# Kernel optimization log

Hardware: AMD Instinct MI355X
Metric: run time of the kernel (lower is better)

Reference implementation:

```python
import jax, jax.numpy as jnp
import numpy as np
import math

DIM = 2048
N_HEADS = 16
HEAD_DIM = DIM // N_HEADS  # 128
SEQ = 2048
EPS = 1e-5
NEG = -1e9


def get_slopes(n):
    # n is a power of 2 here (16)
    start = 2.0 ** (-2.0 ** (-(math.log2(n) - 3)))
    return [start * start ** i for i in range(n)]


def setup_inputs() -> dict:
    key = jax.random.key(0)
    ks = jax.random.split(key, 6)
    x = jax.random.normal(ks[0], (1, SEQ, DIM), dtype=jnp.float32)
    # causal additive mask (large negative above diagonal)
    causal = jnp.tril(jnp.ones((SEQ, SEQ), dtype=bool))
    mask = jnp.where(causal, 0.0, NEG).astype(jnp.float32)[None, None]
    scale_w = 0.02
    wq = jax.random.normal(ks[1], (DIM, DIM), dtype=jnp.float32) * scale_w  # [in, out]
    wk = jax.random.normal(ks[2], (DIM, DIM), dtype=jnp.float32) * scale_w
    wv = jax.random.normal(ks[3], (DIM, DIM), dtype=jnp.float32) * scale_w
    wo = jax.random.normal(ks[4], (DIM, DIM), dtype=jnp.float32) * scale_w
    # AttentionPrior params: shape_init=1, scale_init='slope' (stored as log), loc_init=0
    shape = jnp.ones((1, N_HEADS, 1, 1), dtype=jnp.float32)
    scale = jnp.log(jnp.asarray(get_slopes(N_HEADS), dtype=jnp.float32)).reshape(1, N_HEADS, 1, 1)
    loc = jnp.zeros((1, N_HEADS, 1, 1), dtype=jnp.float32)
    return {"x": x, "mask": mask, "wq": wq, "wk": wk, "wv": wv, "wo": wo,
            "shape": shape, "scale": scale, "loc": loc, "start_pos": 0}


def _prior_bias(shape, scale, loc, seqlen, start_pos):
    q_pos = jnp.arange(seqlen, dtype=jnp.float32) + start_pos
    k_pos = jnp.arange(seqlen + start_pos, dtype=jnp.float32)
    dist = (k_pos[None, :] - q_pos[:, None])[None, None]  # [1,1,S,K]
    loc_t = jnp.exp(loc) - jnp.exp(-loc)
    z = (dist - loc_t) * jnp.exp(scale)  # [1,H,S,K]
    return -(jnp.abs(z) + EPS) ** shape


def reference(x, mask, wq, wk, wv, wo, shape, scale, loc, start_pos):
    bsz, seqlen, _ = x.shape
    q = (x @ wq).reshape(bsz, seqlen, N_HEADS, HEAD_DIM)
    k = (x @ wk).reshape(bsz, seqlen, N_HEADS, HEAD_DIM)
    v = (x @ wv).reshape(bsz, seqlen, N_HEADS, HEAD_DIM)
    # start_pos=0 prefill: cache slice == current keys/values
    scores = jnp.einsum('bqhd,bkhd->bhqk', q, k) / math.sqrt(HEAD_DIM)
    scores = scores + _prior_bias(shape, scale, loc, seqlen, start_pos)
    scores = scores + mask
    probs = jax.nn.softmax(scores.astype(jnp.float32), axis=-1).astype(q.dtype)
    out = jnp.einsum('bhqk,bkhd->bqhd', probs, v).reshape(bsz, seqlen, DIM)
    return out @ wo
```

## Files before the change

kernel.cpp:

```cpp
#include <hip/hip_runtime.h>
#include <hip/hip_bf16.h>
#include <stdint.h>


typedef unsigned short u16;
typedef unsigned int u32;

using bf16x8 = __attribute__((ext_vector_type(8))) __bf16;
using f32x4  = __attribute__((ext_vector_type(4))) float;

__device__ __forceinline__ u16 f2bf(float f) {
  union { float f; u32 u; } v; v.f = f;
  u32 r = (v.u + 0x7FFFu + ((v.u >> 16) & 1u)) >> 16;
  return (u16)r;
}

__device__ __forceinline__ void gload16(const void* g, void* l) {
  __builtin_amdgcn_global_load_lds((const __attribute__((address_space(1))) void*)g,
                                   (__attribute__((address_space(3))) void*)l, 16, 0, 0);
}

__device__ __forceinline__ int cumchunks(int qt) {
  if (qt < 8)  return qt;
  if (qt < 16) return 8 + 2 * (qt - 8);
  if (qt < 24) return 24 + 3 * (qt - 16);
  return 48 + 4 * (qt - 24);
}

__global__ __launch_bounds__(256) void convx(const float* __restrict__ x, u16* __restrict__ xb) {
  int i = blockIdx.x * 256 + threadIdx.x;
  float4 v = ((const float4*)x)[i];
  ushort4 o;
  o.x = f2bf(v.x); o.y = f2bf(v.y); o.z = f2bf(v.z); o.w = f2bf(v.w);
  ((ushort4*)xb)[i] = o;
}

__global__ __launch_bounds__(256) void transw(const float* __restrict__ wq, const float* __restrict__ wk,
                                              const float* __restrict__ wv, const float* __restrict__ wo,
                                              u16* __restrict__ wqkt, u16* __restrict__ wvt,
                                              u16* __restrict__ wot) {
  __shared__ float tile[32][33];
  const int z = blockIdx.z;
  const float* src = (z == 0) ? wq : (z == 1) ? wk : (z == 2) ? wv : wo;
  u16* dst = (z == 0) ? wqkt : (z == 1) ? (wqkt + 2048 * 2048) : (z == 2) ? wvt : wot;
  const int c0 = blockIdx.x * 32, r0 = blockIdx.y * 32;
  const int t = threadIdx.x;
  const int ci = t & 31, rj = t >> 5;
#pragma unroll
  for (int j = 0; j < 4; ++j)
    tile[rj + j * 8][ci] = src[(size_t)(r0 + rj + j * 8) * 2048 + c0 + ci];
  __syncthreads();
#pragma unroll
  for (int j = 0; j < 4; ++j) {
    int rr = rj + j * 8;
    dst[(size_t)(c0 + rr) * 2048 + r0 + ci] = f2bf(tile[ci][rr]);
  }
}

template <int OUTF32>
__global__ __launch_bounds__(256) void gemm_bt(const u16* __restrict__ A, const u16* __restrict__ Bt,
                                               void* __restrict__ Cv, int M, int N, int K,
                                               float scl, int scl_cols) {
  __shared__ u16 lds[16384];
  const int t = threadIdx.x;
  const int w = t >> 6, l = t & 63;
  const int bn = blockIdx.x, bm = blockIdx.y;
  const int wm = w >> 1, wn = w & 1;
  const int lrow = l & 15, lgrp = l >> 4;

  f32x4 acc[4][4] = {};

  for (int k0 = 0; k0 < K; k0 += 64) {
    if (k0) __syncthreads();
#pragma unroll
    for (int p = 0; p < 4; ++p) {
      int i = (p * 4 + w) * 64 + l;
      int r = i >> 3, u = i & 7;
      const u16* src = A + (size_t)(bm * 128 + r) * K + k0 + ((u ^ (r & 7)) << 3);
      gload16(src, (char*)lds + (p * 4 + w) * 1024);
    }
#pragma unroll
    for (int p = 0; p < 4; ++p) {
      int i = (p * 4 + w) * 64 + l;
      int r = i >> 3, u = i & 7;
      const u16* src = Bt + (size_t)(bn * 128 + r) * K + k0 + ((u ^ (r & 7)) << 3);
      gload16(src, (char*)lds + 16384 + (p * 4 + w) * 1024);
    }
    __syncthreads();

#pragma unroll
    for (int kc = 0; kc < 2; ++kc) {
      bf16x8 af[4], bfr[4];
#pragma unroll
      for (int mt = 0; mt < 4; ++mt) {
        int rho = wm * 64 + mt * 16 + lrow;
        int un = (kc * 4 + lgrp) ^ (rho & 7);
        af[mt] = *(const bf16x8*)((const char*)lds + rho * 128 + un * 16);
      }
#pragma unroll
      for (int nt = 0; nt < 4; ++nt) {
        int rho = wn * 64 + nt * 16 + lrow;
        int un = (kc * 4 + lgrp) ^ (rho & 7);
        bfr[nt] = *(const bf16x8*)((const char*)lds + 16384 + rho * 128 + un * 16);
      }
#pragma unroll
      for (int mt = 0; mt < 4; ++mt)
#pragma unroll
        for (int nt = 0; nt < 4; ++nt)
          acc[mt][nt] = __builtin_amdgcn_mfma_f32_16x16x32_bf16(af[mt], bfr[nt], acc[mt][nt], 0, 0, 0);
    }
  }

  const int row0 = bm * 128 + wm * 64;
  const int col0 = bn * 128 + wn * 64;
#pragma unroll
  for (int mt = 0; mt < 4; ++mt)
#pragma unroll
    for (int nt = 0; nt < 4; ++nt) {
      int col = col0 + nt * 16 + lrow;
      float s = (col < scl_cols) ? scl : 1.0f;
#pragma unroll
      for (int r = 0; r < 4; ++r) {
        int row = row0 + mt * 16 + lgrp * 4 + r;
        float v = acc[mt][nt][r] * s;
        if (OUTF32) ((float*)Cv)[(size_t)row * N + col] = v;
        else        ((u16*)Cv)[(size_t)row * N + col] = f2bf(v);
      }
    }
}

__global__ __launch_bounds__(256) void attn_part(const u16* __restrict__ QK, const u16* __restrict__ Vt,
                                                 float* __restrict__ Opart, float* __restrict__ Lpart,
                                                 const float* __restrict__ g_shape,
                                                 const float* __restrict__ g_scale,
                                                 const float* __restrict__ g_loc,
                                                 const int* __restrict__ g_sp) {
  __shared__ u16 k_lds[2][8192];
  __shared__ u16 v_lds[2][8192];
  __shared__ u16 p_lds[4][1152];

  const int bid = blockIdx.x;
  const int h = bid / 80;
  const int rem = bid - h * 80;
  int qt, ch;
  if (rem < 8)       { qt = rem;                 ch = 0; }
  else if (rem < 24) { int r2 = rem - 8;  qt = 8  + (r2 >> 1); ch = r2 & 1; }
  else if (rem < 48) { int r3 = rem - 24; qt = 16 + r3 / 3;    ch = r3 - 3 * (r3 / 3); }
  else               { int r4 = rem - 48; qt = 24 + (r4 >> 2); ch = r4 & 3; }
  const int pid = bid;

  const int t = threadIdx.x, w = t >> 6, l = t & 63;
  const int lrow = l & 15, lgrp = l >> 4;

  const float sh = g_shape[h];
  const float es = __expf(g_scale[h]);
  const float lcv = g_loc[h];
  const float loc_t = __expf(lcv) - __expf(-lcv);
  const int sp = g_sp[0];
  const bool shape1 = (sh == 1.0f);

  const int qbase = qt * 64 + w * 16;

  bf16x8 qf[4];
  {
    const u16* qp = QK + (size_t)(qbase + lrow) * 4096 + h * 128 + lgrp * 8;
#pragma unroll
    for (int kc = 0; kc < 4; ++kc) qf[kc] = *(const bf16x8*)(qp + kc * 32);
  }

  f32x4 o[8] = {};
  float lr[4] = {0.0f, 0.0f, 0.0f, 0.0f};

  const int kstart = ch * 8;
  const int kend = min(kstart + 8, qt + 1);

#define STAGE_TILE(buf, kt_) do {                                                        \
    const int kv0s = (kt_) * 64;                                                         \
    _Pragma("unroll")                                                                    \
    for (int p = 0; p < 4; ++p) {                                                        \
      int i = (p * 4 + w) * 64 + l;                                                      \
      int r = i >> 4, u = i & 15;                                                        \
      const u16* src = QK + (size_t)(kv0s + r) * 4096 + 2048 + h * 128 + ((u ^ (r & 7)) << 3); \
      gload16(src, (char*)k_lds[buf] + (p * 4 + w) * 1024);                              \
    }                                                                                    \
    _Pragma("unroll")                                                                    \
    for (int p = 0; p < 4; ++p) {                                                        \
      int i = (p * 4 + w) * 64 + l;                                                      \
      int r = i >> 3, u = i & 7;                                                         \
      const u16* src = Vt + (size_t)(h * 128 + r) * 2048 + kv0s + ((u ^ (r & 7)) << 3);  \
      gload16(src, (char*)v_lds[buf] + (p * 4 + w) * 1024);                              \
    }                                                                                    \
  } while (0)

  STAGE_TILE(0, kstart);
  __syncthreads();

  for (int kt = kstart; kt < kend; ++kt) {
    const int cur = (kt - kstart) & 1;
    if (kt + 1 < kend) STAGE_TILE(cur ^ 1, kt + 1);
    const int kv0 = kt * 64;

    f32x4 s4[4];
#pragma unroll
    for (int nc = 0; nc < 4; ++nc) s4[nc] = f32x4{-11.0f, -11.0f, -11.0f, -11.0f};
#pragma unroll
    for (int kc = 0; kc < 4; ++kc) {
#pragma unroll
      for (int nc = 0; nc < 4; ++nc) {
        int rho = nc * 16 + lrow;
        int un = (kc * 4 + lgrp) ^ (rho & 7);
        bf16x8 bk = *(const bf16x8*)((const char*)k_lds[cur] + rho * 256 + un * 16);
        s4[nc] = __builtin_amdgcn_mfma_f32_16x16x32_bf16(qf[kc], bk, s4[nc], 0, 0, 0);
      }
    }

    f32x4 p4[4];
    const bool need_mask = (kv0 + 63 > qbase + sp);
    if (shape1 && !need_mask) {
#pragma unroll
      for (int r = 0; r < 4; ++r) {
        const float fb = (float)(kv0 + lrow - (qbase + lgrp * 4 + r) - sp) - loc_t;
#pragma unroll
        for (int nc = 0; nc < 4; ++nc) {
          float u = fb + (float)(nc * 16);
          float p = __expf(fmaf(-es, fabsf(u), s4[nc][r]));
          p4[nc][r] = p;
          lr[r] += p;
        }
      }
    } else if (shape1) {
#pragma unroll
      for (int r = 0; r < 4; ++r) {
        const float fb = (float)(kv0 + lrow - (qbase + lgrp * 4 + r) - sp) - loc_t;
#pragma unroll
        for (int nc = 0; nc < 4; ++nc) {
          float u = fb + (float)(nc * 16);
          float p = __expf(fmaf(-es, fabsf(u), s4[nc][r]));
          p = (u + loc_t > 0.0f) ? 0.0f : p;
          p4[nc][r] = p;
          lr[r] += p;
        }
      }
    } else {
#pragma unroll
      for (int r = 0; r < 4; ++r) {
        const float fb = (float)(kv0 + lrow - (qbase + lgrp * 4 + r) - sp) - loc_t;
#pragma unroll
        for (int nc = 0; nc < 4; ++nc) {
          float u = fb + (float)(nc * 16);
          float az = fmaf(es, fabsf(u), 1e-5f);
          float p = __expf(s4[nc][r] - __powf(az, sh));
          p = (u + loc_t > 0.0f) ? 0.0f : p;
          p4[nc][r] = p;
          lr[r] += p;
        }
      }
    }

#pragma unroll
    for (int r = 0; r < 4; ++r)
#pragma unroll
      for (int nc = 0; nc < 4; ++nc)
        p_lds[w][(lgrp * 4 + r) * 72 + nc * 16 + lrow] = f2bf(p4[nc][r]);

#pragma unroll
    for (int ks = 0; ks < 2; ++ks) {
      bf16x8 pa = *(const bf16x8*)((const char*)p_lds[w] + lrow * 144 + ks * 64 + lgrp * 16);
#pragma unroll
      for (int dc = 0; dc < 8; ++dc) {
        int rho = dc * 16 + lrow;
        int un = (ks * 4 + lgrp) ^ (rho & 7);
        bf16x8 bv = *(const bf16x8*)((const char*)v_lds[cur] + rho * 128 + un * 16);
        o[dc] = __builtin_amdgcn_mfma_f32_16x16x32_bf16(pa, bv, o[dc], 0, 0, 0);
      }
    }

    __syncthreads();
  }
#undef STAGE_TILE

#pragma unroll
  for (int r = 0; r < 4; ++r)
#pragma unroll
    for (int msk = 1; msk <= 8; msk <<= 1) lr[r] += __shfl_xor(lr[r], msk);

  float* ob = Opart + (size_t)pid * 8192;
#pragma unroll
  for (int dc = 0; dc < 8; ++dc) {
#pragma unroll
    for (int r = 0; r < 4; ++r) {
      int row = w * 16 + lgrp * 4 + r;
      ob[(size_t)row * 128 + dc * 16 + lrow] = o[dc][r];
    }
  }
  if (lrow == 0) {
#pragma unroll
    for (int r = 0; r < 4; ++r) {
      int row = w * 16 + lgrp * 4 + r;
      Lpart[(size_t)pid * 64 + row] = lr[r];
    }
  }
}

__global__ __launch_bounds__(256) void attn_merge(const float* __restrict__ Opart,
                                                  const float* __restrict__ Lpart,
                                                  u16* __restrict__ AO) {
  const int bid = blockIdx.x;
  const int qt = bid & 31, h = bid >> 5;
  const int nch = (qt >> 3) + 1;
  const int base = h * 80 + cumchunks(qt);
  const int t = threadIdx.x;
  const int row = t >> 2;
  const int dseg = (t & 3) << 5;

  float4 acc[8] = {};
  float lstar = 0.0f;
#pragma unroll
  for (int i = 0; i < 4; ++i) {
    if (i < nch) {
      lstar += Lpart[(size_t)(base + i) * 64 + row];
      const float4* op = (const float4*)(Opart + (size_t)(base + i) * 8192 + row * 128 + dseg);
#pragma unroll
      for (int j = 0; j < 8; ++j) {
        float4 v = op[j];
        acc[j].x += v.x; acc[j].y += v.y;
        acc[j].z += v.z; acc[j].w += v.w;
      }
    }
  }
  const float inv = 1.0f / lstar;
  const int q_abs = qt * 64 + row;
  u16* dst = AO + (size_t)q_abs * 2048 + h * 128 + dseg;
#pragma unroll
  for (int j = 0; j < 8; ++j) {
    ushort4 ov;
    ov.x = f2bf(acc[j].x * inv); ov.y = f2bf(acc[j].y * inv);
    ov.z = f2bf(acc[j].z * inv); ov.w = f2bf(acc[j].w * inv);
    *(ushort4*)(dst + j * 4) = ov;
  }
}

extern "C" void kernel_launch(void* const* d_in, const int* in_sizes, int n_in,
                              void* d_out, int out_size, void* d_ws, size_t ws_size,
                              hipStream_t stream) {
  const float* x   = (const float*)d_in[0];
  const float* wq  = (const float*)d_in[2];
  const float* wk  = (const float*)d_in[3];
  const float* wv  = (const float*)d_in[4];
  const float* wo  = (const float*)d_in[5];
  const float* shp = (const float*)d_in[6];
  const float* scl = (const float*)d_in[7];
  const float* loc = (const float*)d_in[8];
  const int*   sp  = (const int*)d_in[9];

  char* ws = (char*)d_ws;
  u16*   xb    = (u16*)(ws);
  u16*   wqkt  = (u16*)(ws + (size_t)( 8u << 20));
  u16*   wvt   = (u16*)(ws + (size_t)(24u << 20));
  float* opart = (float*)(ws);
  u16*   wot   = (u16*)(ws + (size_t)(40u << 20));
  u16*   qk    = (u16*)(ws + (size_t)(48u << 20));
  u16*   vt    = (u16*)(ws + (size_t)(64u << 20));
  u16*   ao    = (u16*)(ws + (size_t)(72u << 20));
  float* lpart = (float*)(ws + (size_t)(80u << 20));

  hipLaunchKernelGGL(convx, dim3(4096), dim3(256), 0, stream, x, xb);
  hipLaunchKernelGGL(transw, dim3(64, 64, 4), dim3(256), 0, stream, wq, wk, wv, wo, wqkt, wvt, wot);
  hipLaunchKernelGGL((gemm_bt<0>), dim3(32, 16), dim3(256), 0, stream,
                     xb, wqkt, (void*)qk, 2048, 4096, 2048, 0.08838834764831843f, 2048);
  hipLaunchKernelGGL((gemm_bt<0>), dim3(16, 16), dim3(256), 0, stream,
                     wvt, xb, (void*)vt, 2048, 2048, 2048, 1.0f, 0);
  hipLaunchKernelGGL(attn_part, dim3(1280), dim3(256), 0, stream,
                     qk, vt, opart, lpart, shp, scl, loc, sp);
  hipLaunchKernelGGL(attn_merge, dim3(512), dim3(256), 0, stream, opart, lpart, ao);
  hipLaunchKernelGGL((gemm_bt<1>), dim3(16, 16), dim3(256), 0, stream,
                     ao, wot, (void*)d_out, 2048, 2048, 2048, 1.0f, 0);
}
```

Before: 201.3 us.

## Merge QK and V projection GEMMs into one launch; store attention partials in bf16

Fuses the two projection GEMMs (QK with 512 tiles, V-transposed with 256 tiles) into a single 768-block launch. This fills the GPU better and removes one launch and its tail. It also stores the per-chunk attention partial outputs as bf16 instead of fp32, halving the write/read traffic between attn_part and attn_merge. The cost is some precision loss in the unnormalized partial sums before merging.

```diff
diff --git a/kernel.cpp b/kernel.cpp
--- a/kernel.cpp
+++ b/kernel.cpp
@@ -13,6 +13,10 @@
   union { float f; u32 u; } v; v.f = f;
   u32 r = (v.u + 0x7FFFu + ((v.u >> 16) & 1u)) >> 16;
   return (u16)r;
+}
+
+__device__ __forceinline__ float bf2f(u16 h) {
+  union { u32 u; float f; } v; v.u = ((u32)h) << 16; return v.f;
 }
 
 __device__ __forceinline__ void gload16(const void* g, void* l) {
@@ -57,10 +61,84 @@
   }
 }
 
-template <int OUTF32>
-__global__ __launch_bounds__(256) void gemm_bt(const u16* __restrict__ A, const u16* __restrict__ Bt,
-                                               void* __restrict__ Cv, int M, int N, int K,
-                                               float scl, int scl_cols) {
+__global__ __launch_bounds__(256) void gemm_qkv(const u16* __restrict__ xb, const u16* __restrict__ wqkt,
+                                                const u16* __restrict__ wvt,
+                                                u16* __restrict__ qkc, u16* __restrict__ vtc) {
+  __shared__ u16 lds[16384];
+  int bid = blockIdx.x;
+  const u16 *A, *Bt;
+  u16* C;
+  int N, bn, bm, scl_cols;
+  if (bid < 512) { A = xb;  Bt = wqkt; C = qkc; N = 4096; bn = bid & 31; bm = bid >> 5; scl_cols = 2048; }
+  else { bid -= 512; A = wvt; Bt = xb; C = vtc; N = 2048; bn = bid & 15; bm = bid >> 4; scl_cols = 0; }
+  const int K = 2048;
+
+  const int t = threadIdx.x;
+  const int w = t >> 6, l = t & 63;
+  const int wm = w >> 1, wn = w & 1;
+  const int lrow = l & 15, lgrp = l >> 4;
+
+  f32x4 acc[4][4] = {};
+
+  for (int k0 = 0; k0 < K; k0 += 64) {
+    if (k0) __syncthreads();
+#pragma unroll
+    for (int p = 0; p < 4; ++p) {
+      int i = (p * 4 + w) * 64 + l;
+      int r = i >> 3, u = i & 7;
+      const u16* src = A + (size_t)(bm * 128 + r) * K + k0 + ((u ^ (r & 7)) << 3);
+      gload16(src, (char*)lds + (p * 4 + w) * 1024);
+    }
+#pragma unroll
+    for (int p = 0; p < 4; ++p) {
+      int i = (p * 4 + w) * 64 + l;
+      int r = i >> 3, u = i & 7;
+      const u16* src = Bt + (size_t)(bn * 128 + r) * K + k0 + ((u ^ (r & 7)) << 3);
+      gload16(src, (char*)lds + 16384 + (p * 4 + w) * 1024);
+    }
+    __syncthreads();
+
+#pragma unroll
+    for (int kc = 0; kc < 2; ++kc) {
+      bf16x8 af[4], bfr[4];
+#pragma unroll
+      for (int mt = 0; mt < 4; ++mt) {
+        int rho = wm * 64 + mt * 16 + lrow;
+        int un = (kc * 4 + lgrp) ^ (rho & 7);
+        af[mt] = *(const bf16x8*)((const char*)lds + rho * 128 + un * 16);
+      }
+#pragma unroll
+      for (int nt = 0; nt < 4; ++nt) {
+        int rho = wn * 64 + nt * 16 + lrow;
+        int un = (kc * 4 + lgrp) ^ (rho & 7);
+        bfr[nt] = *(const bf16x8*)((const char*)lds + 16384 + rho * 128 + un * 16);
+      }
+#pragma unroll
+      for (int mt = 0; mt < 4; ++mt)
+#pragma unroll
+        for (int nt = 0; nt < 4; ++nt)
+          acc[mt][nt] = __builtin_amdgcn_mfma_f32_16x16x32_bf16(af[mt], bfr[nt], acc[mt][nt], 0, 0, 0);
+    }
+  }
+
+  const int row0 = bm * 128 + wm * 64;
+  const int col0 = bn * 128 + wn * 64;
+#pragma unroll
+  for (int mt = 0; mt < 4; ++mt)
+#pragma unroll
+    for (int nt = 0; nt < 4; ++nt) {
+      int col = col0 + nt * 16 + lrow;
+      float s = (col < scl_cols) ? 0.08838834764831843f : 1.0f;
+#pragma unroll
+      for (int r = 0; r < 4; ++r) {
+        int row = row0 + mt * 16 + lgrp * 4 + r;
+        C[(size_t)row * N + col] = f2bf(acc[mt][nt][r] * s);
+      }
+    }
+}
+
+__global__ __launch_bounds__(256) void gemm_out(const u16* __restrict__ A, const u16* __restrict__ Bt,
+                                                float* __restrict__ Cv, int M, int N, int K) {
   __shared__ u16 lds[16384];
   const int t = threadIdx.x;
   const int w = t >> 6, l = t & 63;
@@ -118,19 +196,16 @@
 #pragma unroll
     for (int nt = 0; nt < 4; ++nt) {
       int col = col0 + nt * 16 + lrow;
-      float s = (col < scl_cols) ? scl : 1.0f;
 #pragma unroll
       for (int r = 0; r < 4; ++r) {
         int row = row0 + mt * 16 + lgrp * 4 + r;
-        float v = acc[mt][nt][r] * s;
-        if (OUTF32) ((float*)Cv)[(size_t)row * N + col] = v;
-        else        ((u16*)Cv)[(size_t)row * N + col] = f2bf(v);
+        Cv[(size_t)row * N + col] = acc[mt][nt][r];
       }
     }
 }
 
 __global__ __launch_bounds__(256) void attn_part(const u16* __restrict__ QK, const u16* __restrict__ Vt,
-                                                 float* __restrict__ Opart, float* __restrict__ Lpart,
+                                                 u16* __restrict__ Opart, float* __restrict__ Lpart,
                                                  const float* __restrict__ g_shape,
                                                  const float* __restrict__ g_scale,
                                                  const float* __restrict__ g_loc,
@@ -284,13 +359,13 @@
 #pragma unroll
     for (int msk = 1; msk <= 8; msk <<= 1) lr[r] += __shfl_xor(lr[r], msk);
 
-  float* ob = Opart + (size_t)pid * 8192;
+  u16* ob = Opart + (size_t)pid * 8192;
 #pragma unroll
   for (int dc = 0; dc < 8; ++dc) {
 #pragma unroll
     for (int r = 0; r < 4; ++r) {
       int row = w * 16 + lgrp * 4 + r;
-      ob[(size_t)row * 128 + dc * 16 + lrow] = o[dc][r];
+      ob[(size_t)row * 128 + dc * 16 + lrow] = f2bf(o[dc][r]);
     }
   }
   if (lrow == 0) {
@@ -302,7 +377,7 @@
   }
 }
 
-__global__ __launch_bounds__(256) void attn_merge(const float* __restrict__ Opart,
+__global__ __launch_bounds__(256) void attn_merge(const u16* __restrict__ Opart,
                                                   const float* __restrict__ Lpart,
                                                   u16* __restrict__ AO) {
   const int bid = blockIdx.x;
@@ -313,18 +388,18 @@
   const int row = t >> 2;
   const int dseg = (t & 3) << 5;
 
-  float4 acc[8] = {};
+  float acc[32] = {};
   float lstar = 0.0f;
 #pragma unroll
   for (int i = 0; i < 4; ++i) {
     if (i < nch) {
       lstar += Lpart[(size_t)(base + i) * 64 + row];
-      const float4* op = (const float4*)(Opart + (size_t)(base + i) * 8192 + row * 128 + dseg);
+      const ushort4* op = (const ushort4*)(Opart + (size_t)(base + i) * 8192 + row * 128 + dseg);
 #pragma unroll
       for (int j = 0; j < 8; ++j) {
-        float4 v = op[j];
-        acc[j].x += v.x; acc[j].y += v.y;
-        acc[j].z += v.z; acc[j].w += v.w;
+        ushort4 v = op[j];
+        acc[j * 4 + 0] += bf2f(v.x); acc[j * 4 + 1] += bf2f(v.y);
+        acc[j * 4 + 2] += bf2f(v.z); acc[j * 4 + 3] += bf2f(v.w);
       }
     }
   }
@@ -334,8 +409,8 @@
 #pragma unroll
   for (int j = 0; j < 8; ++j) {
     ushort4 ov;
-    ov.x = f2bf(acc[j].x * inv); ov.y = f2bf(acc[j].y * inv);
-    ov.z = f2bf(acc[j].z * inv); ov.w = f2bf(acc[j].w * inv);
+    ov.x = f2bf(acc[j * 4 + 0] * inv); ov.y = f2bf(acc[j * 4 + 1] * inv);
+    ov.z = f2bf(acc[j * 4 + 2] * inv); ov.w = f2bf(acc[j * 4 + 3] * inv);
     *(ushort4*)(dst + j * 4) = ov;
   }
 }
@@ -357,7 +432,7 @@
   u16*   xb    = (u16*)(ws);
   u16*   wqkt  = (u16*)(ws + (size_t)( 8u << 20));
   u16*   wvt   = (u16*)(ws + (size_t)(24u << 20));
-  float* opart = (float*)(ws);
+  u16*   opart = (u16*)(ws);
   u16*   wot   = (u16*)(ws + (size_t)(40u << 20));
   u16*   qk    = (u16*)(ws + (size_t)(48u << 20));
   u16*   vt    = (u16*)(ws + (size_t)(64u << 20));
@@ -366,13 +441,10 @@
 
   hipLaunchKernelGGL(convx, dim3(4096), dim3(256), 0, stream, x, xb);
   hipLaunchKernelGGL(transw, dim3(64, 64, 4), dim3(256), 0, stream, wq, wk, wv, wo, wqkt, wvt, wot);
-  hipLaunchKernelGGL((gemm_bt<0>), dim3(32, 16), dim3(256), 0, stream,
-                     xb, wqkt, (void*)qk, 2048, 4096, 2048, 0.08838834764831843f, 2048);
-  hipLaunchKernelGGL((gemm_bt<0>), dim3(16, 16), dim3(256), 0, stream,
-                     wvt, xb, (void*)vt, 2048, 2048, 2048, 1.0f, 0);
+  hipLaunchKernelGGL(gemm_qkv, dim3(768), dim3(256), 0, stream, xb, wqkt, wvt, qk, vt);
   hipLaunchKernelGGL(attn_part, dim3(1280), dim3(256), 0, stream,
                      qk, vt, opart, lpart, shp, scl, loc, sp);
   hipLaunchKernelGGL(attn_merge, dim3(512), dim3(256), 0, stream, opart, lpart, ao);
-  hipLaunchKernelGGL((gemm_bt<1>), dim3(16, 16), dim3(256), 0, stream,
-                     ao, wot, (void*)d_out, 2048, 2048, 2048, 1.0f, 0);
-}
+  hipLaunchKernelGGL(gemm_out, dim3(16, 16), dim3(256), 0, stream,
+                     ao, wot, (float*)d_out, 2048, 2048, 2048);
+}
```

After: 177.7 us. 1.13x faster.
